# Optimization experiments

Hardware: AMD Instinct MI355X
Metric: run time of the kernel (lower is better)

## Reference

```python
import jax, jax.numpy as jnp
import numpy as np

N = 1_500_000
NUM_VOXELS = 262_144  # static segment count (replaces torch.unique's dynamic voxel count)
VSIZE = np.array([0.32, 0.32, 0.32], np.float32)
PC_MIN = np.array([-74.88, -74.88, -2.0], np.float32)
GRID = np.array([468, 468, 32], np.int64)
BN_EPS = 1e-3


def setup_inputs() -> dict:
    rng = np.random.default_rng(0)
    # points uniformly inside the point-cloud range -> the range mask is all-true
    xyz = rng.uniform(PC_MIN, PC_MIN + VSIZE * GRID - 1e-3, size=(N, 3)).astype(np.float32)
    feats = rng.uniform(0.0, 1.0, size=(N, 1)).astype(np.float32)
    coords = np.floor((xyz - PC_MIN) / VSIZE).astype(np.int64)
    merge = coords[:, 0] * (GRID[1] * GRID[2]) + coords[:, 1] * GRID[2] + coords[:, 2]
    unq_inv = (merge % NUM_VOXELS).astype(np.int32)  # static-size stand-in for unique inverse ids
    key = jax.random.key(0)
    k1, k2 = jax.random.split(key)
    return {
        'points_xyz': jnp.asarray(xyz),
        'point_feats': jnp.asarray(feats),
        'w1': jax.random.normal(k1, (11, 32), jnp.float32) * 0.1,
        'g1': jnp.ones((32,), jnp.float32),
        'b1': jnp.zeros((32,), jnp.float32),
        'w2': jax.random.normal(k2, (64, 64), jnp.float32) * 0.1,
        'g2': jnp.ones((64,), jnp.float32),
        'b2': jnp.zeros((64,), jnp.float32),
        'unq_inv': jnp.asarray(unq_inv),
    }


def _pfn(x, w, g, b, unq_inv):
    # Linear(bias=False) -> BatchNorm1d(train-mode batch stats, eps=1e-3) -> ReLU -> scatter_max
    y = x @ w
    mu = jnp.mean(y, axis=0)
    var = jnp.var(y, axis=0)
    y = (y - mu) * jax.lax.rsqrt(var + BN_EPS) * g + b
    y = jax.nn.relu(y)
    # relu output >= 0; clamp empty segments (-inf) to 0, matching torch_scatter's zero fill
    y_max = jnp.maximum(jax.ops.segment_max(y, unq_inv, num_segments=NUM_VOXELS), 0.0)
    return y, y_max


def reference(points_xyz, point_feats, w1, g1, b1, w2, g2, b2, unq_inv):
    vsize = jnp.asarray(VSIZE)
    pc_min = jnp.asarray(PC_MIN)
    coords = jnp.floor((points_xyz - pc_min) / vsize)  # [N,3] float voxel coords

    # scatter_mean of xyz per voxel -> cluster-relative offsets
    ones = jnp.ones((points_xyz.shape[0],), points_xyz.dtype)
    cnt = jax.ops.segment_sum(ones, unq_inv, num_segments=NUM_VOXELS)
    vsum = jax.ops.segment_sum(points_xyz, unq_inv, num_segments=NUM_VOXELS)
    vmean = vsum / jnp.maximum(cnt, 1.0)[:, None]
    f_cluster = points_xyz - vmean[unq_inv]

    # offset from voxel center
    f_center = points_xyz - (coords * vsize + vsize * 0.5 + pc_min)
    dist = jnp.linalg.norm(points_xyz, axis=1, keepdims=True)

    feat = jnp.concatenate([points_xyz, point_feats, f_cluster, f_center, dist], axis=-1)  # [N,11]

    x, x_max = _pfn(feat, w1, g1, b1, unq_inv)            # [N,32], [V,32]
    x = jnp.concatenate([x, x_max[unq_inv]], axis=1)       # [N,64]
    _, out = _pfn(x, w2, g2, b2, unq_inv)                  # [V,64] pillar features
    return out
```

## Files before the change

kernel.cpp:

```cpp
#include <hip/hip_runtime.h>

#define NPTS 1500000
#define NVOX 262144
#define BN_EPS 1e-3f
#define PAD 1500160
#define NB_PT 5860
#define NB_L2 11720

typedef __attribute__((ext_vector_type(8))) short bf16x8;
typedef __attribute__((ext_vector_type(4))) float f32x4;

__device__ __forceinline__ unsigned fkey(float f) {
    unsigned u = __float_as_uint(f);
    return u ^ ((unsigned)(((int)u) >> 31) | 0x80000000u);
}
__device__ __forceinline__ float funkey(unsigned k) {
    unsigned u = (k & 0x80000000u) ? (k ^ 0x80000000u) : ~k;
    return __uint_as_float(u);
}
#define KEY_NEG_INF 0x007FFFFFu

__device__ __forceinline__ float bf2f(unsigned short h) {
    union { unsigned u; float f; } x; x.u = ((unsigned)h) << 16; return x.f;
}
__device__ __forceinline__ unsigned short f2bf(float f) {
    union { float f; unsigned u; } x; x.f = f;
    unsigned r = x.u + 0x7FFFu + ((x.u >> 16) & 1u);
    return (unsigned short)(r >> 16);
}
__device__ __forceinline__ unsigned packbf(float a, float b) {
    return (unsigned)f2bf(a) | ((unsigned)f2bf(b) << 16);
}

__device__ __forceinline__ void make_feat(float x, float y, float z, float w,
                                          float mx, float my, float mz, float* f) {
    const float VS = 0.32f;
    const float PMX = -74.88f, PMY = -74.88f, PMZ = -2.0f;
    f[0] = x; f[1] = y; f[2] = z; f[3] = w;
    f[4] = x - mx; f[5] = y - my; f[6] = z - mz;
    float cx = floorf((x - PMX) / VS);
    float cy = floorf((y - PMY) / VS);
    float cz = floorf((z - PMZ) / VS);
    f[7] = x - (cx * VS + 0.5f * VS + PMX);
    f[8] = y - (cy * VS + 0.5f * VS + PMY);
    f[9] = z - (cz * VS + 0.5f * VS + PMZ);
    f[10] = sqrtf(x * x + y * y + z * z);
}

__global__ void k_init(unsigned* __restrict__ okeys, unsigned* __restrict__ xmraw,
                       int* __restrict__ cntv, float* __restrict__ zf,
                       int* __restrict__ svid, const float* __restrict__ w2,
                       uint4* __restrict__ wfrag) {
    long t0 = (long)blockIdx.x * 256 + threadIdx.x;
    long st = (long)gridDim.x * 256;
    uint4 kneg = make_uint4(KEY_NEG_INF, KEY_NEG_INF, KEY_NEG_INF, KEY_NEG_INF);
    for (long i = t0; i < (long)NVOX * 16; i += st) ((uint4*)okeys)[i] = kneg;
    for (long i = t0; i < (long)NVOX * 8; i += st) ((uint4*)xmraw)[i] = kneg;
    for (long i = t0; i < NVOX / 4; i += st) ((int4*)cntv)[i] = make_int4(0, 0, 0, 0);
    for (long i = t0; i < (1024 + 256 * 64 + 256 * 128) / 4; i += st)
        ((float4*)zf)[i] = make_float4(0.f, 0.f, 0.f, 0.f);
    if (t0 < PAD - NPTS) svid[NPTS + t0] = -1;
    if (blockIdx.x == 0 && threadIdx.x < 64) {
        int l = threadIdx.x;
        int lr = l & 15, lk = l >> 4;
        #pragma unroll
        for (int nt = 0; nt < 4; ++nt)
            #pragma unroll
            for (int kt = 0; kt < 2; ++kt) {
                int col = nt * 16 + lr;
                int kb = kt * 32 + lk * 8;
                unsigned u[4];
                #pragma unroll
                for (int j = 0; j < 4; ++j) {
                    float a = w2[(kb + 2 * j) * 64 + col];
                    float b = w2[(kb + 2 * j + 1) * 64 + col];
                    u[j] = packbf(a, b);
                }
                wfrag[(nt * 2 + kt) * 64 + l] = make_uint4(u[0], u[1], u[2], u[3]);
            }
    }
}

__global__ void k_hist(const int* __restrict__ unq, int* __restrict__ cntv) {
    int i = blockIdx.x * blockDim.x + threadIdx.x;
    if (i < NPTS) atomicAdd(&cntv[unq[i]], 1);
}

__global__ void k_scanA(const int* __restrict__ cntv, int* __restrict__ startv,
                        int* __restrict__ bsum) {
    __shared__ int lds[256];
    int t = threadIdx.x;
    int idx4 = blockIdx.x * 256 + t;
    int4 cv = ((const int4*)cntv)[idx4];
    int s0 = cv.x, s1 = s0 + cv.y, s2 = s1 + cv.z, T = s2 + cv.w;
    lds[t] = T;
    __syncthreads();
    for (int o = 1; o < 256; o <<= 1) {
        int v = (t >= o) ? lds[t - o] : 0;
        __syncthreads();
        lds[t] += v;
        __syncthreads();
    }
    int excl = lds[t] - T;
    int4 ov; ov.x = excl; ov.y = excl + s0; ov.z = excl + s1; ov.w = excl + s2;
    ((int4*)startv)[idx4] = ov;
    if (t == 255) bsum[blockIdx.x] = lds[255];
}

__global__ void k_scanB(int* __restrict__ bsum) {
    __shared__ int lds[256];
    int t = threadIdx.x;
    int b = bsum[t];
    lds[t] = b;
    __syncthreads();
    for (int o = 1; o < 256; o <<= 1) {
        int v = (t >= o) ? lds[t - o] : 0;
        __syncthreads();
        lds[t] += v;
        __syncthreads();
    }
    bsum[t] = lds[t] - b;
}

__global__ void k_scanC(int* __restrict__ startv, int* __restrict__ offv,
                        const int* __restrict__ bsum) {
    int t = threadIdx.x;
    int idx4 = blockIdx.x * 256 + t;
    int add = bsum[blockIdx.x];
    int4 v = ((int4*)startv)[idx4];
    v.x += add; v.y += add; v.z += add; v.w += add;
    ((int4*)startv)[idx4] = v;
    ((int4*)offv)[idx4] = v;
}

__global__ void k_scatter2(const float* __restrict__ xyz, const float* __restrict__ pf,
                           const int* __restrict__ unq, int* __restrict__ offv,
                           float4* __restrict__ spts, int* __restrict__ svid) {
    int i = blockIdx.x * blockDim.x + threadIdx.x;
    if (i >= NPTS) return;
    int v = unq[i];
    int pos = atomicAdd(&offv[v], 1);
    float4 p;
    p.x = xyz[3 * i + 0]; p.y = xyz[3 * i + 1]; p.z = xyz[3 * i + 2]; p.w = pf[i];
    spts[pos] = p;
    svid[pos] = v;
}

__global__ void k_vmean2(const float4* __restrict__ spts, const int* __restrict__ cntv,
                         const int* __restrict__ startv, float4* __restrict__ vmeanv) {
    int v = blockIdx.x * 256 + threadIdx.x;
    int cnt = cntv[v];
    if (!cnt) return;
    int st = startv[v];
    float sx = 0, sy = 0, sz = 0;
    for (int j = 0; j < cnt; ++j) {
        float4 p = spts[st + j];
        sx += p.x; sy += p.y; sz += p.z;
    }
    float inv = 1.0f / (float)cnt;
    vmeanv[v] = make_float4(sx * inv, sy * inv, sz * inv, 0.f);
}

__device__ __forceinline__ void flush32(int v, float m, bool atom, int c,
                                        unsigned* __restrict__ xm) {
    if ((unsigned)v >= (unsigned)NVOX) return;
    if (atom) atomicMax(&xm[(size_t)v * 32 + c], fkey(m));
    else xm[(size_t)v * 32 + c] = fkey(m);
}
__device__ __forceinline__ void flush64(int v, float m, bool atom, int c,
                                        unsigned* __restrict__ ok) {
    if ((unsigned)v >= (unsigned)NVOX) return;
    if (atom) atomicMax(&ok[(size_t)v * 64 + c], fkey(m));
    else ok[(size_t)v * 64 + c] = fkey(m);
}

__global__ __launch_bounds__(256) void k_passA(
    const float4* __restrict__ spts, const int* __restrict__ svid,
    const float4* __restrict__ vmeanv, const float* __restrict__ w1,
    unsigned* __restrict__ xmraw, float* __restrict__ spart1) {
    __shared__ float ylds[4][32 * 33];
    int t = threadIdx.x;
    int lane = t & 63, wave = t >> 6;
    int rl = lane & 31, half = lane >> 5;
    long grow = (long)blockIdx.x * 128 + wave * 32 + rl;
    int vid = svid[grow];
    float yv[16];
    #pragma unroll
    for (int j = 0; j < 16; ++j) yv[j] = 0.f;
    if (vid >= 0) {
        float4 p = spts[grow];
        float4 vm = vmeanv[vid];
        float f[11];
        make_feat(p.x, p.y, p.z, p.w, vm.x, vm.y, vm.z, f);
        const float4* w1f = (const float4*)w1;
        #pragma unroll
        for (int k = 0; k < 11; ++k) {
            float fk = f[k];
            #pragma unroll
            for (int q = 0; q < 4; ++q) {
                float4 wq = w1f[k * 8 + half * 4 + q];
                yv[4 * q + 0] = fmaf(fk, wq.x, yv[4 * q + 0]);
                yv[4 * q + 1] = fmaf(fk, wq.y, yv[4 * q + 1]);
                yv[4 * q + 2] = fmaf(fk, wq.z, yv[4 * q + 2]);
                yv[4 * q + 3] = fmaf(fk, wq.w, yv[4 * q + 3]);
            }
        }
    }
    float* yw = &ylds[wave][0];
    #pragma unroll
    for (int j = 0; j < 16; ++j) yw[rl * 33 + half * 16 + j] = yv[j];
    asm volatile("s_waitcnt lgkmcnt(0)" ::: "memory");
    __builtin_amdgcn_sched_barrier(0);
    int c = rl;
    float sa = 0.f, sq = 0.f;
    int cur_v = -2; float cur_m = 0.f; bool first = true;
    #pragma unroll
    for (int i = 0; i < 16; ++i) {
        int r = half * 16 + i;
        float y = yw[r * 33 + c];
        int v = __shfl(vid, r);
        sa += y; sq += y * y;
        if (i == 0) { cur_v = v; cur_m = y; }
        else if (v == cur_v) cur_m = fmaxf(cur_m, y);
        else {
            flush32(cur_v, cur_m, first, c, xmraw);
            first = false; cur_v = v; cur_m = y;
        }
    }
    flush32(cur_v, cur_m, true, c, xmraw);
    sa += __shfl_xor(sa, 32);
    sq += __shfl_xor(sq, 32);
    if (half == 0) {
        int slot = (blockIdx.x * 4 + wave) & 255;
        atomicAdd(&spart1[slot * 64 + c], sa);
        atomicAdd(&spart1[slot * 64 + 32 + c], sq);
    }
}

__global__ void k_fin1(const float* __restrict__ spart1, float* __restrict__ stats,
                       const float* __restrict__ g1, const float* __restrict__ b1) {
    __shared__ float cs[64];
    int t = threadIdx.x;
    float s = 0.f;
    for (int r = 0; r < 256; ++r) s += spart1[r * 64 + t];
    cs[t] = s;
    __syncthreads();
    if (t < 32) {
        float invn = 1.0f / (float)NPTS;
        float mu = cs[t] * invn;
        float var = cs[32 + t] * invn - mu * mu;
        float sc = rsqrtf(var + BN_EPS) * g1[t];
        stats[64 + t] = sc;
        stats[96 + t] = b1[t] - mu * sc;
    }
}

__global__ __launch_bounds__(256) void k_l2(
    const float4* __restrict__ spts, const int* __restrict__ svid,
    const float4* __restrict__ vmeanv, const float* __restrict__ w1,
    const unsigned* __restrict__ xmraw, const uint4* __restrict__ wfrag,
    const float* __restrict__ stats, float* __restrict__ spart2,
    unsigned* __restrict__ okeys) {
    __shared__ unsigned Abuf[4][32 * 32];
    __shared__ unsigned y2t[4][64 * 17];
    int t = threadIdx.x;
    int lane = t & 63, wave = t >> 6;
    int rl = lane & 31, half = lane >> 5;
    int lr = lane & 15, lk = lane >> 4;
    long brow = (long)blockIdx.x * 128 + wave * 32;
    int vid = svid[brow + rl];

    unsigned zpk[8], xpk[8];
    if (vid >= 0) {
        float4 p = spts[brow + rl];
        float4 vm = vmeanv[vid];
        float f[11];
        make_feat(p.x, p.y, p.z, p.w, vm.x, vm.y, vm.z, f);
        float yv[16];
        #pragma unroll
        for (int j = 0; j < 16; ++j) yv[j] = 0.f;
        const float4* w1f = (const float4*)w1;
        #pragma unroll
        for (int k = 0; k < 11; ++k) {
            float fk = f[k];
            #pragma unroll
            for (int q = 0; q < 4; ++q) {
                float4 wq = w1f[k * 8 + half * 4 + q];
                yv[4 * q + 0] = fmaf(fk, wq.x, yv[4 * q + 0]);
                yv[4 * q + 1] = fmaf(fk, wq.y, yv[4 * q + 1]);
                yv[4 * q + 2] = fmaf(fk, wq.z, yv[4 * q + 2]);
                yv[4 * q + 3] = fmaf(fk, wq.w, yv[4 * q + 3]);
            }
        }
        const uint4* xr = (const uint4*)(xmraw + (size_t)vid * 32);
        uint4 xq[4];
        #pragma unroll
        for (int q = 0; q < 4; ++q) xq[q] = xr[half * 4 + q];
        const unsigned* xu = (const unsigned*)xq;
        #pragma unroll
        for (int q = 0; q < 4; ++q) {
            float4 sc = ((const float4*)(stats + 64))[half * 4 + q];
            float4 sh = ((const float4*)(stats + 96))[half * 4 + q];
            float z0 = fmaxf(0.f, fmaf(yv[4 * q + 0], sc.x, sh.x));
            float z1 = fmaxf(0.f, fmaf(yv[4 * q + 1], sc.y, sh.y));
            float z2 = fmaxf(0.f, fmaf(yv[4 * q + 2], sc.z, sh.z));
            float z3 = fmaxf(0.f, fmaf(yv[4 * q + 3], sc.w, sh.w));
            zpk[2 * q + 0] = packbf(z0, z1);
            zpk[2 * q + 1] = packbf(z2, z3);
            float x0 = fmaxf(0.f, fmaf(funkey(xu[4 * q + 0]), sc.x, sh.x));
            float x1 = fmaxf(0.f, fmaf(funkey(xu[4 * q + 1]), sc.y, sh.y));
            float x2 = fmaxf(0.f, fmaf(funkey(xu[4 * q + 2]), sc.z, sh.z));
            float x3 = fmaxf(0.f, fmaf(funkey(xu[4 * q + 3]), sc.w, sh.w));
            xpk[2 * q + 0] = packbf(x0, x1);
            xpk[2 * q + 1] = packbf(x2, x3);
        }
    } else {
        #pragma unroll
        for (int q = 0; q < 8; ++q) { zpk[q] = 0u; xpk[q] = 0u; }
    }
    {
        uint4* arow = (uint4*)&Abuf[wave][rl * 32];
        int sw = rl & 7;
        arow[(2 * half + 0) ^ sw] = *(const uint4*)&zpk[0];
        arow[(2 * half + 1) ^ sw] = *(const uint4*)&zpk[4];
        arow[(4 + 2 * half) ^ sw] = *(const uint4*)&xpk[0];
        arow[(5 + 2 * half) ^ sw] = *(const uint4*)&xpk[4];
    }
    asm volatile("s_waitcnt lgkmcnt(0)" ::: "memory");
    __builtin_amdgcn_sched_barrier(0);

    uint4 bw[8];
    #pragma unroll
    for (int q = 0; q < 8; ++q) bw[q] = wfrag[q * 64 + lane];

    bf16x8 afr[2][2];
    #pragma unroll
    for (int mt = 0; mt < 2; ++mt)
        #pragma unroll
        for (int kt = 0; kt < 2; ++kt) {
            int riw = mt * 16 + lr;
            uint4 uu = ((const uint4*)&Abuf[wave][riw * 32])[(kt * 4 + lk) ^ (riw & 7)];
            afr[mt][kt] = __builtin_bit_cast(bf16x8, uu);
        }
    f32x4 acc[2][4];
    #pragma unroll
    for (int mt = 0; mt < 2; ++mt)
        #pragma unroll
        for (int nt = 0; nt < 4; ++nt) {
            acc[mt][nt] = (f32x4){0.f, 0.f, 0.f, 0.f};
            #pragma unroll
            for (int kt = 0; kt < 2; ++kt)
                acc[mt][nt] = __builtin_amdgcn_mfma_f32_16x16x32_bf16(
                    afr[mt][kt], __builtin_bit_cast(bf16x8, bw[nt * 2 + kt]),
                    acc[mt][nt], 0, 0, 0);
        }

    #pragma unroll
    for (int mt = 0; mt < 2; ++mt)
        #pragma unroll
        for (int nt = 0; nt < 4; ++nt) {
            int col = nt * 16 + lr;
            int w0 = mt * 8 + lk * 2;
            y2t[wave][col * 17 + w0] = packbf(acc[mt][nt][0], acc[mt][nt][1]);
            y2t[wave][col * 17 + w0 + 1] = packbf(acc[mt][nt][2], acc[mt][nt][3]);
        }

    {
        float sa[4] = {0.f, 0.f, 0.f, 0.f}, sq[4] = {0.f, 0.f, 0.f, 0.f};
        #pragma unroll
        for (int mt = 0; mt < 2; ++mt)
            #pragma unroll
            for (int nt = 0; nt < 4; ++nt)
                #pragma unroll
                for (int e = 0; e < 4; ++e) {
                    float v = acc[mt][nt][e];
                    sa[nt] += v; sq[nt] += v * v;
                }
        #pragma unroll
        for (int nt = 0; nt < 4; ++nt) {
            sa[nt] += __shfl_xor(sa[nt], 16); sa[nt] += __shfl_xor(sa[nt], 32);
            sq[nt] += __shfl_xor(sq[nt], 16); sq[nt] += __shfl_xor(sq[nt], 32);
        }
        if (lk == 0) {
            int slot = (blockIdx.x * 4 + wave) & 255;
            #pragma unroll
            for (int nt = 0; nt < 4; ++nt) {
                atomicAdd(&spart2[slot * 128 + nt * 16 + lr], sa[nt]);
                atomicAdd(&spart2[slot * 128 + 64 + nt * 16 + lr], sq[nt]);
            }
        }
    }
    asm volatile("s_waitcnt lgkmcnt(0)" ::: "memory");
    __builtin_amdgcn_sched_barrier(0);

    {
        int c = lane;
        int cur_v = -2; float cur_m = 0.f; bool first = true;
        #pragma unroll
        for (int q = 0; q < 16; ++q) {
            unsigned u = y2t[wave][c * 17 + q];
            #pragma unroll
            for (int e = 0; e < 2; ++e) {
                float d = bf2f((unsigned short)(e ? (u >> 16) : (u & 0xFFFF)));
                int v = __shfl(vid, 2 * q + e);
                if (q == 0 && e == 0) { cur_v = v; cur_m = d; }
                else if (v == cur_v) cur_m = fmaxf(cur_m, d);
                else {
                    flush64(cur_v, cur_m, first, c, okeys);
                    first = false; cur_v = v; cur_m = d;
                }
            }
        }
        flush64(cur_v, cur_m, true, c, okeys);
    }
}

__global__ void k_fin2(const float* __restrict__ spart2, float* __restrict__ stats,
                       const float* __restrict__ g2, const float* __restrict__ b2) {
    __shared__ float cs[128];
    int t = threadIdx.x;
    float s = 0.f;
    for (int r = 0; r < 256; ++r) s += spart2[r * 128 + t];
    cs[t] = s;
    __syncthreads();
    if (t < 64) {
        float invn = 1.0f / (float)NPTS;
        float mu = cs[t] * invn;
        float var = cs[64 + t] * invn - mu * mu;
        float sc = rsqrtf(var + BN_EPS) * g2[t];
        stats[256 + t] = sc;
        stats[320 + t] = b2[t] - mu * sc;
    }
}

__global__ void k_out(unsigned* __restrict__ okeys, const float* __restrict__ stats) {
    int i4 = blockIdx.x * 256 + threadIdx.x;
    uint4 u = ((const uint4*)okeys)[i4];
    int c0 = (i4 & 15) * 4;
    float4 o;
    o.x = fmaxf(0.f, fmaf(funkey(u.x), stats[256 + c0 + 0], stats[320 + c0 + 0]));
    o.y = fmaxf(0.f, fmaf(funkey(u.y), stats[256 + c0 + 1], stats[320 + c0 + 1]));
    o.z = fmaxf(0.f, fmaf(funkey(u.z), stats[256 + c0 + 2], stats[320 + c0 + 2]));
    o.w = fmaxf(0.f, fmaf(funkey(u.w), stats[256 + c0 + 3], stats[320 + c0 + 3]));
    ((float4*)okeys)[i4] = o;
}

extern "C" void kernel_launch(void* const* d_in, const int* in_sizes, int n_in,
                              void* d_out, int out_size, void* d_ws, size_t ws_size,
                              hipStream_t stream) {
    const float* xyz = (const float*)d_in[0];
    const float* pf  = (const float*)d_in[1];
    const float* w1  = (const float*)d_in[2];
    const float* g1  = (const float*)d_in[3];
    const float* b1  = (const float*)d_in[4];
    const float* w2  = (const float*)d_in[5];
    const float* g2  = (const float*)d_in[6];
    const float* b2  = (const float*)d_in[7];
    const int*   unq = (const int*)d_in[8];

    float4* spts     = (float4*)d_ws;
    float4* vmeanv   = spts + PAD;
    int* svid        = (int*)(vmeanv + NVOX);
    unsigned* xmraw  = (unsigned*)(svid + PAD);
    int* cntv        = (int*)(xmraw + (size_t)NVOX * 32);
    int* startv      = cntv + NVOX;
    int* offv        = startv + NVOX;
    int* bsum        = offv + NVOX;
    float* stats     = (float*)(bsum + 256);
    float* spart1    = stats + 1024;
    float* spart2    = spart1 + 256 * 64;
    uint4* wfrag     = (uint4*)(spart2 + 256 * 128);

    unsigned* okeys = (unsigned*)d_out;

    k_init<<<2048, 256, 0, stream>>>(okeys, xmraw, cntv, stats, svid, w2, wfrag);
    k_hist<<<NB_PT, 256, 0, stream>>>(unq, cntv);
    k_scanA<<<256, 256, 0, stream>>>(cntv, startv, bsum);
    k_scanB<<<1, 256, 0, stream>>>(bsum);
    k_scanC<<<256, 256, 0, stream>>>(startv, offv, bsum);
    k_scatter2<<<NB_PT, 256, 0, stream>>>(xyz, pf, unq, offv, spts, svid);
    k_vmean2<<<NVOX / 256, 256, 0, stream>>>(spts, cntv, startv, vmeanv);
    k_passA<<<NB_L2, 256, 0, stream>>>(spts, svid, vmeanv, w1, xmraw, spart1);
    k_fin1<<<1, 64, 0, stream>>>(spart1, stats, g1, b1);
    k_l2<<<NB_L2, 256, 0, stream>>>(spts, svid, vmeanv, w1, xmraw, wfrag, stats,
                                    spart2, okeys);
    k_fin2<<<1, 128, 0, stream>>>(spart2, stats, g2, b2);
    k_out<<<NVOX * 16 / 256, 256, 0, stream>>>(okeys, stats);
}
```

Measured before the change: 430.4 us.

## Cache layer-1 pre-BN outputs as bf16 instead of recomputing in layer 2

Pass A now writes the 32-channel layer-1 linear output per point to a bf16 buffer. Layer 2 reads it back instead of reloading points and voxel means and recomputing the features and the 11x32 matmul. The change also merges the two LDS buffers in layer 2 into one to cut shared-memory use, and moves the weight-fragment load earlier. The trade is extra global traffic (about 64 B per point written and read) against less compute and fewer gathers, with some added bf16 rounding on the pre-BN values.

```diff
diff --git a/kernel.cpp b/kernel.cpp
--- a/kernel.cpp
+++ b/kernel.cpp
@@ -177,7 +177,8 @@
 __global__ __launch_bounds__(256) void k_passA(
     const float4* __restrict__ spts, const int* __restrict__ svid,
     const float4* __restrict__ vmeanv, const float* __restrict__ w1,
-    unsigned* __restrict__ xmraw, float* __restrict__ spart1) {
+    unsigned* __restrict__ xmraw, unsigned* __restrict__ y1bf,
+    float* __restrict__ spart1) {
     __shared__ float ylds[4][32 * 33];
     int t = threadIdx.x;
     int lane = t & 63, wave = t >> 6;
@@ -205,6 +206,14 @@
                 yv[4 * q + 3] = fmaf(fk, wq.w, yv[4 * q + 3]);
             }
         }
+    }
+    {
+        unsigned ypk[8];
+        #pragma unroll
+        for (int q = 0; q < 8; ++q) ypk[q] = packbf(yv[2 * q], yv[2 * q + 1]);
+        uint4* yb = (uint4*)y1bf;
+        yb[grow * 4 + half * 2 + 0] = *(const uint4*)&ypk[0];
+        yb[grow * 4 + half * 2 + 1] = *(const uint4*)&ypk[4];
     }
     float* yw = &ylds[wave][0];
     #pragma unroll
@@ -256,13 +265,11 @@
 }
 
 __global__ __launch_bounds__(256) void k_l2(
-    const float4* __restrict__ spts, const int* __restrict__ svid,
-    const float4* __restrict__ vmeanv, const float* __restrict__ w1,
+    const int* __restrict__ svid, const unsigned* __restrict__ y1bf,
     const unsigned* __restrict__ xmraw, const uint4* __restrict__ wfrag,
     const float* __restrict__ stats, float* __restrict__ spart2,
     unsigned* __restrict__ okeys) {
-    __shared__ unsigned Abuf[4][32 * 32];
-    __shared__ unsigned y2t[4][64 * 17];
+    __shared__ unsigned shbuf[4][1088];
     int t = threadIdx.x;
     int lane = t & 63, wave = t >> 6;
     int rl = lane & 31, half = lane >> 5;
@@ -270,43 +277,32 @@
     long brow = (long)blockIdx.x * 128 + wave * 32;
     int vid = svid[brow + rl];
 
+    uint4 bw[8];
+    #pragma unroll
+    for (int q = 0; q < 8; ++q) bw[q] = wfrag[q * 64 + lane];
+    uint4 yu0 = ((const uint4*)y1bf)[(brow + rl) * 4 + half * 2];
+    uint4 yu1 = ((const uint4*)y1bf)[(brow + rl) * 4 + half * 2 + 1];
+
     unsigned zpk[8], xpk[8];
     if (vid >= 0) {
-        float4 p = spts[brow + rl];
-        float4 vm = vmeanv[vid];
-        float f[11];
-        make_feat(p.x, p.y, p.z, p.w, vm.x, vm.y, vm.z, f);
-        float yv[16];
-        #pragma unroll
-        for (int j = 0; j < 16; ++j) yv[j] = 0.f;
-        const float4* w1f = (const float4*)w1;
-        #pragma unroll
-        for (int k = 0; k < 11; ++k) {
-            float fk = f[k];
-            #pragma unroll
-            for (int q = 0; q < 4; ++q) {
-                float4 wq = w1f[k * 8 + half * 4 + q];
-                yv[4 * q + 0] = fmaf(fk, wq.x, yv[4 * q + 0]);
-                yv[4 * q + 1] = fmaf(fk, wq.y, yv[4 * q + 1]);
-                yv[4 * q + 2] = fmaf(fk, wq.z, yv[4 * q + 2]);
-                yv[4 * q + 3] = fmaf(fk, wq.w, yv[4 * q + 3]);
-            }
-        }
         const uint4* xr = (const uint4*)(xmraw + (size_t)vid * 32);
         uint4 xq[4];
         #pragma unroll
         for (int q = 0; q < 4; ++q) xq[q] = xr[half * 4 + q];
         const unsigned* xu = (const unsigned*)xq;
+        unsigned yw[8] = {yu0.x, yu0.y, yu0.z, yu0.w, yu1.x, yu1.y, yu1.z, yu1.w};
         #pragma unroll
         for (int q = 0; q < 4; ++q) {
             float4 sc = ((const float4*)(stats + 64))[half * 4 + q];
             float4 sh = ((const float4*)(stats + 96))[half * 4 + q];
-            float z0 = fmaxf(0.f, fmaf(yv[4 * q + 0], sc.x, sh.x));
-            float z1 = fmaxf(0.f, fmaf(yv[4 * q + 1], sc.y, sh.y));
-            float z2 = fmaxf(0.f, fmaf(yv[4 * q + 2], sc.z, sh.z));
-            float z3 = fmaxf(0.f, fmaf(yv[4 * q + 3], sc.w, sh.w));
-            zpk[2 * q + 0] = packbf(z0, z1);
-            zpk[2 * q + 1] = packbf(z2, z3);
+            float yA = bf2f((unsigned short)(yw[2 * q] & 0xFFFF));
+            float yB = bf2f((unsigned short)(yw[2 * q] >> 16));
+            float yC = bf2f((unsigned short)(yw[2 * q + 1] & 0xFFFF));
+            float yD = bf2f((unsigned short)(yw[2 * q + 1] >> 16));
+            zpk[2 * q + 0] = packbf(fmaxf(0.f, fmaf(yA, sc.x, sh.x)),
+                                    fmaxf(0.f, fmaf(yB, sc.y, sh.y)));
+            zpk[2 * q + 1] = packbf(fmaxf(0.f, fmaf(yC, sc.z, sh.z)),
+                                    fmaxf(0.f, fmaf(yD, sc.w, sh.w)));
             float x0 = fmaxf(0.f, fmaf(funkey(xu[4 * q + 0]), sc.x, sh.x));
             float x1 = fmaxf(0.f, fmaf(funkey(xu[4 * q + 1]), sc.y, sh.y));
             float x2 = fmaxf(0.f, fmaf(funkey(xu[4 * q + 2]), sc.z, sh.z));
@@ -319,7 +315,7 @@
         for (int q = 0; q < 8; ++q) { zpk[q] = 0u; xpk[q] = 0u; }
     }
     {
-        uint4* arow = (uint4*)&Abuf[wave][rl * 32];
+        uint4* arow = (uint4*)&shbuf[wave][rl * 32];
         int sw = rl & 7;
         arow[(2 * half + 0) ^ sw] = *(const uint4*)&zpk[0];
         arow[(2 * half + 1) ^ sw] = *(const uint4*)&zpk[4];
@@ -329,19 +325,18 @@
     asm volatile("s_waitcnt lgkmcnt(0)" ::: "memory");
     __builtin_amdgcn_sched_barrier(0);
 
-    uint4 bw[8];
-    #pragma unroll
-    for (int q = 0; q < 8; ++q) bw[q] = wfrag[q * 64 + lane];
-
     bf16x8 afr[2][2];
     #pragma unroll
     for (int mt = 0; mt < 2; ++mt)
         #pragma unroll
         for (int kt = 0; kt < 2; ++kt) {
             int riw = mt * 16 + lr;
-            uint4 uu = ((const uint4*)&Abuf[wave][riw * 32])[(kt * 4 + lk) ^ (riw & 7)];
+            uint4 uu = ((const uint4*)&shbuf[wave][riw * 32])[(kt * 4 + lk) ^ (riw & 7)];
             afr[mt][kt] = __builtin_bit_cast(bf16x8, uu);
         }
+    asm volatile("s_waitcnt lgkmcnt(0)" ::: "memory");
+    __builtin_amdgcn_sched_barrier(0);
+
     f32x4 acc[2][4];
     #pragma unroll
     for (int mt = 0; mt < 2; ++mt)
@@ -355,14 +350,15 @@
                     acc[mt][nt], 0, 0, 0);
         }
 
+    unsigned* y2w = &shbuf[wave][0];
     #pragma unroll
     for (int mt = 0; mt < 2; ++mt)
         #pragma unroll
         for (int nt = 0; nt < 4; ++nt) {
             int col = nt * 16 + lr;
             int w0 = mt * 8 + lk * 2;
-            y2t[wave][col * 17 + w0] = packbf(acc[mt][nt][0], acc[mt][nt][1]);
-            y2t[wave][col * 17 + w0 + 1] = packbf(acc[mt][nt][2], acc[mt][nt][3]);
+            y2w[col * 17 + w0] = packbf(acc[mt][nt][0], acc[mt][nt][1]);
+            y2w[col * 17 + w0 + 1] = packbf(acc[mt][nt][2], acc[mt][nt][3]);
         }
 
     {
@@ -398,7 +394,7 @@
         int cur_v = -2; float cur_m = 0.f; bool first = true;
         #pragma unroll
         for (int q = 0; q < 16; ++q) {
-            unsigned u = y2t[wave][c * 17 + q];
+            unsigned u = y2w[c * 17 + q];
             #pragma unroll
             for (int e = 0; e < 2; ++e) {
                 float d = bf2f((unsigned short)(e ? (u >> 16) : (u & 0xFFFF)));
@@ -470,6 +466,7 @@
     float* spart1    = stats + 1024;
     float* spart2    = spart1 + 256 * 64;
     uint4* wfrag     = (uint4*)(spart2 + 256 * 128);
+    unsigned* y1bf   = (unsigned*)(wfrag + 512);
 
     unsigned* okeys = (unsigned*)d_out;
 
@@ -480,10 +477,9 @@
     k_scanC<<<256, 256, 0, stream>>>(startv, offv, bsum);
     k_scatter2<<<NB_PT, 256, 0, stream>>>(xyz, pf, unq, offv, spts, svid);
     k_vmean2<<<NVOX / 256, 256, 0, stream>>>(spts, cntv, startv, vmeanv);
-    k_passA<<<NB_L2, 256, 0, stream>>>(spts, svid, vmeanv, w1, xmraw, spart1);
+    k_passA<<<NB_L2, 256, 0, stream>>>(spts, svid, vmeanv, w1, xmraw, y1bf, spart1);
     k_fin1<<<1, 64, 0, stream>>>(spart1, stats, g1, b1);
-    k_l2<<<NB_L2, 256, 0, stream>>>(spts, svid, vmeanv, w1, xmraw, wfrag, stats,
-                                    spart2, okeys);
+    k_l2<<<NB_L2, 256, 0, stream>>>(svid, y1bf, xmraw, wfrag, stats, spart2, okeys);
     k_fin2<<<1, 128, 0, stream>>>(spart2, stats, g2, b2);
     k_out<<<NVOX * 16 / 256, 256, 0, stream>>>(okeys, stats);
 }
```

After: 391.7 us. 9.0% less time.
